# Kernel optimization log

Measured on AMD Instinct MI355X. Metric: run time of the kernel, lower is better.

The kernel has to match this reference:

```python
import jax, jax.numpy as jnp
import numpy as np

DIM = 512
WINDOW = 8
HEADS = 16
HEAD_DIM = DIM // HEADS
SIGMA = 0.39
B = 2048
N = WINDOW * WINDOW


def gaussian_kernel(window_size, sigma):
    """Row-normalised Gaussian attention mask K_sigma (M^2 x M^2)."""
    c = jnp.arange(window_size, dtype=jnp.float32)
    gy, gx = jnp.meshgrid(c, c, indexing='ij')
    pos = jnp.stack([gy.flatten(), gx.flatten()], -1)  # [M^2, 2]
    diff = pos[None, :, :] - pos[:, None, :]           # [M^2, M^2, 2]
    K = jnp.exp(-(diff ** 2).sum(-1) / (2.0 * sigma ** 2))
    return K / K.sum(-1, keepdims=True)


def setup_inputs() -> dict:
    key = jax.random.key(0)
    k1, k2, k3, k4, k5 = jax.random.split(key, 5)
    x = jax.random.normal(k1, (B, N, DIM), dtype=jnp.float32)
    # spectral_norm at inference is just a fixed scaling of the weight; we
    # model the (already-normalised) weights as plain dense params.
    w_qkv = jax.random.normal(k2, (DIM, 3 * DIM), dtype=jnp.float32) * (DIM ** -0.5)
    b_qkv = jax.random.normal(k3, (3 * DIM,), dtype=jnp.float32) * 0.02
    w_proj = jax.random.normal(k4, (DIM, DIM), dtype=jnp.float32) * (DIM ** -0.5)
    b_proj = jax.random.normal(k5, (DIM,), dtype=jnp.float32) * 0.02
    return {"x": x, "w_qkv": w_qkv, "b_qkv": b_qkv, "w_proj": w_proj, "b_proj": b_proj}


def reference(x, w_qkv, b_qkv, w_proj, b_proj):
    Bb, Nn, C = x.shape
    scale = HEAD_DIM ** -0.5
    qkv = (x @ w_qkv + b_qkv).reshape(Bb, Nn, 3, HEADS, HEAD_DIM)
    qkv = jnp.transpose(qkv, (2, 0, 3, 1, 4))  # [3, B, H, N, D]
    q, k, v = qkv[0], qkv[1], qkv[2]
    attn = jnp.einsum('bhnd,bhmd->bhnm', q, k) * scale  # [B, H, N, N]
    K_s = gaussian_kernel(WINDOW, SIGMA)                 # [N, N]
    attn = jax.nn.softmax(attn * K_s, axis=-1)
    out = jnp.einsum('bhnm,bhmd->bhnd', attn, v)         # [B, H, N, D]
    out = jnp.transpose(out, (0, 2, 1, 3)).reshape(Bb, Nn, C)
    return out @ w_proj + b_proj
```

## Files before the change

### kernel.cpp

```cpp
#include <hip/hip_runtime.h>
#include <hip/hip_bf16.h>
#include <stdint.h>

typedef __bf16 bf16;
typedef __bf16 bf16x8 __attribute__((ext_vector_type(8)));
typedef float f32x4 __attribute__((ext_vector_type(4)));
typedef unsigned short u16t;
typedef unsigned int u32t;

#define MFMA16(a, b, c) __builtin_amdgcn_mfma_f32_16x16x32_bf16((a), (b), (c), 0, 0, 0)

typedef const void __attribute__((address_space(1))) cg_void;
typedef void __attribute__((address_space(3))) lds_void;
#define GLL16(g, l) __builtin_amdgcn_global_load_lds((cg_void*)(g), (lds_void*)(l), 16, 0, 0)
#define VWAIT(n) asm volatile("s_waitcnt vmcnt(" #n ")" ::: "memory")

#define OFF_FLAG   0
#define OFF_BQKV   256
#define OFF_BPROJ  6400
#define OFF_WQKVT  8448
#define OFF_WPROJT 1581312
#define OFF_QKV    2105600
#define OFF_ATTN   404758784
#define OFF_XB     404758784

__global__ __launch_bounds__(256) void k_detect(const u16t* x, u32t* flag) {
    __shared__ int cnt;
    if (threadIdx.x == 0) cnt = 0;
    __syncthreads();
    u16t h = x[threadIdx.x * 2];
    int e = (h >> 7) & 0xFF;
    int ok = (h == 0) || (e >= 100 && e <= 134);
    atomicAdd(&cnt, ok);
    __syncthreads();
    if (threadIdx.x == 0) flag[0] = (cnt >= 200) ? 1u : 0u;
}

__global__ __launch_bounds__(256) void k_cvt(const float* x, bf16* xb, const u32t* flagp) {
    if (flagp[0]) return;
    const size_t TOT = (size_t)131072 * 512;
    size_t i = (size_t)(blockIdx.x * 256 + threadIdx.x) * 8;
    const size_t stride = (size_t)gridDim.x * 256 * 8;
    for (; i < TOT; i += stride) {
        float4 v0 = *(const float4*)(x + i);
        float4 v1 = *(const float4*)(x + i + 4);
        bf16x8 h;
        h[0] = (bf16)v0.x; h[1] = (bf16)v0.y; h[2] = (bf16)v0.z; h[3] = (bf16)v0.w;
        h[4] = (bf16)v1.x; h[5] = (bf16)v1.y; h[6] = (bf16)v1.z; h[7] = (bf16)v1.w;
        *(bf16x8*)(xb + i) = h;
    }
}

template <int N>
__global__ __launch_bounds__(256) void k_trans(const void* W, bf16* Wt, const u32t* flagp) {
    __shared__ float T[64][65];
    const int isbf = (int)flagp[0];
    const int n0 = blockIdx.x * 64, k0 = blockIdx.y * 64;
    const int t = threadIdx.x;
    const int lc = t & 63, lr = t >> 6;
#pragma unroll
    for (int rr = 0; rr < 16; ++rr) {
        int row = rr * 4 + lr;
        size_t g = (size_t)(k0 + row) * N + n0 + lc;
        float v = isbf ? (float)((const bf16*)W)[g] : ((const float*)W)[g];
        T[row][lc] = v;
    }
    __syncthreads();
#pragma unroll
    for (int rr = 0; rr < 16; ++rr) {
        int row = rr * 4 + lr;
        Wt[(size_t)(n0 + row) * 512 + k0 + lc] = (bf16)T[lc][row];
    }
}

__global__ __launch_bounds__(256) void k_bias(const void* b_qkv, const void* b_proj,
                                              const u32t* flagp, char* ws) {
    float* bq = (float*)(ws + OFF_BQKV);
    float* bp = (float*)(ws + OFF_BPROJ);
    const int isbf = (int)flagp[0];
    int gid = blockIdx.x * 256 + threadIdx.x;
    if (gid < 1536)
        bq[gid] = isbf ? (float)((const bf16*)b_qkv)[gid] : ((const float*)b_qkv)[gid];
    else if (gid < 2048) {
        int o = gid - 1536;
        bp[o] = isbf ? (float)((const bf16*)b_proj)[o] : ((const float*)b_proj)[o];
    }
}

template <int NTOT>
__global__ __launch_bounds__(512, 2) void k_gemm(const void* Ax, const bf16* Axb, const bf16* Bt,
                                                 const float* bias, void* Cp,
                                                 const u32t* flagp, int omode) {
    __shared__ __align__(16) u16t As[2 * 16384];
    __shared__ __align__(16) u16t Bs[2 * 16384];
    constexpr int NBN = NTOT / 256;
    const int isbf = (int)flagp[0];
    const int out_bf16 = (omode == 1) || isbf;
    const bf16* Ab = isbf ? (const bf16*)Ax : Axb;

    const int t = threadIdx.x;
    const int w = t >> 6, lane = t & 63;
    const int ln = lane & 15, qd = lane >> 4;
    const int wm = w >> 2, wn = w & 3;

    const int flat = blockIdx.x;
    const int xcd = flat & 7, slot = flat >> 3;
    const int n_idx = slot % NBN, grp = slot / NBN;
    const int m0 = (grp * 8 + xcd) * 256;
    const int n0 = n_idx * 256;

    const int l8 = lane >> 3, pc = lane & 7;
    const int cs8 = (pc ^ l8) * 8;
    u32t aoff[2][2], boff[2][2];
    int adst[2][2], bdst[2][2];
#pragma unroll
    for (int s = 0; s < 2; ++s)
#pragma unroll
        for (int q2 = 0; q2 < 2; ++q2) {
            int rA = q2 * 128 + s * 64 + w * 8;
            aoff[s][q2] = (u32t)(m0 + rA + l8) * 512 + cs8;
            adst[s][q2] = rA * 64;
            int rB = (q2 * 2 + (w >> 2)) * 64 + s * 32 + (w & 3) * 8;
            boff[s][q2] = (u32t)(n0 + rB + l8) * 512 + cs8;
            bdst[s][q2] = rB * 64;
        }

    const int p0 = (qd ^ (ln & 7)) * 8;
    int abase[4], bbase[2];
#pragma unroll
    for (int i = 0; i < 4; ++i) abase[i] = (wm * 128 + i * 16 + ln) * 64 + p0;
#pragma unroll
    for (int j = 0; j < 2; ++j) bbase[j] = (wn * 64 + j * 16 + ln) * 64 + p0;

    f32x4 acc[8][4];
    f32x4 zero = {0.f, 0.f, 0.f, 0.f};
#pragma unroll
    for (int i = 0; i < 8; ++i)
#pragma unroll
        for (int j = 0; j < 4; ++j) acc[i][j] = zero;

    auto stageA = [&](int s, int buf, int kt) {
#pragma unroll
        for (int q2 = 0; q2 < 2; ++q2)
            GLL16(Ab + aoff[s][q2] + kt * 64, &As[buf * 16384 + adst[s][q2]]);
    };
    auto stageB = [&](int s, int buf, int kt) {
#pragma unroll
        for (int q2 = 0; q2 < 2; ++q2)
            GLL16(Bt + boff[s][q2] + kt * 64, &Bs[buf * 16384 + bdst[s][q2]]);
    };

#define PH(BUF, QM, QN, STG, WAITOP)                                             \
    {                                                                            \
        bf16x8 af[4][2], bv[2][2];                                               \
        const u16t* Ap = &As[(BUF) * 16384 + (QM) * 4096];                       \
        const u16t* Bp = &Bs[(BUF) * 16384 + (QN) * 2048];                       \
        _Pragma("unroll") for (int i = 0; i < 4; ++i) {                          \
            af[i][0] = *(const bf16x8*)(const void*)&Ap[abase[i]];               \
            af[i][1] = *(const bf16x8*)(const void*)&Ap[abase[i] ^ 32];          \
        }                                                                        \
        _Pragma("unroll") for (int j = 0; j < 2; ++j) {                          \
            bv[j][0] = *(const bf16x8*)(const void*)&Bp[bbase[j]];               \
            bv[j][1] = *(const bf16x8*)(const void*)&Bp[bbase[j] ^ 32];          \
        }                                                                        \
        STG;                                                                     \
        WAITOP;                                                                  \
        __builtin_amdgcn_s_barrier();                                            \
        __builtin_amdgcn_s_setprio(1);                                           \
        _Pragma("unroll") for (int i = 0; i < 4; ++i)                            \
            _Pragma("unroll") for (int j = 0; j < 2; ++j) {                      \
                acc[(QM) * 4 + i][(QN) * 2 + j] =                                \
                    MFMA16(af[i][0], bv[j][0], acc[(QM) * 4 + i][(QN) * 2 + j]); \
                acc[(QM) * 4 + i][(QN) * 2 + j] =                                \
                    MFMA16(af[i][1], bv[j][1], acc[(QM) * 4 + i][(QN) * 2 + j]); \
            }                                                                    \
        __builtin_amdgcn_s_setprio(0);                                           \
        __builtin_amdgcn_s_barrier();                                            \
    }

    stageA(0, 0, 0);
    stageB(0, 0, 0);
    stageB(1, 0, 0);
    stageA(1, 0, 0);
    VWAIT(4);
    __builtin_amdgcn_s_barrier();

    for (int kt = 0; kt < 7; ++kt) {
        const int buf = kt & 1, nb = buf ^ 1, k1 = kt + 1;
        PH(buf, 0, 0, stageA(0, nb, k1), VWAIT(4));
        PH(buf, 0, 1, stageB(0, nb, k1), VWAIT(4));
        PH(buf, 1, 0, stageB(1, nb, k1), VWAIT(6));
        PH(buf, 1, 1, stageA(1, nb, k1), VWAIT(4));
    }
    PH(1, 0, 0, (void)0, VWAIT(2));
    PH(1, 0, 1, (void)0, VWAIT(0));
    PH(1, 1, 0, (void)0, (void)0);
    PH(1, 1, 1, (void)0, (void)0);
#undef PH

    float bj[4];
#pragma unroll
    for (int j = 0; j < 4; ++j) bj[j] = bias[n0 + wn * 64 + j * 16 + ln];

    if (out_bf16) {
        bf16* C = (bf16*)Cp;
#pragma unroll
        for (int i = 0; i < 8; ++i)
#pragma unroll
            for (int j = 0; j < 4; ++j)
#pragma unroll
                for (int rr = 0; rr < 4; ++rr) {
                    size_t row = (size_t)m0 + wm * 128 + i * 16 + qd * 4 + rr;
                    int col = n0 + wn * 64 + j * 16 + ln;
                    C[row * NTOT + col] = (bf16)(acc[i][j][rr] + bj[j]);
                }
    } else {
        float* C = (float*)Cp;
#pragma unroll
        for (int i = 0; i < 8; ++i)
#pragma unroll
            for (int j = 0; j < 4; ++j)
#pragma unroll
                for (int rr = 0; rr < 4; ++rr) {
                    size_t row = (size_t)m0 + wm * 128 + i * 16 + qd * 4 + rr;
                    int col = n0 + wn * 64 + j * 16 + ln;
                    C[row * NTOT + col] = acc[i][j][rr] + bj[j];
                }
    }
}

__global__ __launch_bounds__(256) void k_attn(const bf16* qkv, bf16* attn) {
    __shared__ __align__(16) bf16 P[4][64 * 72];
    __shared__ __align__(16) u16t Vs[4][2048];
    const int t = threadIdx.x;
    const int w = t >> 6, lane = t & 63;
    const int ln = lane & 15, qd = lane >> 4, q8 = qd * 8;
    const int flat = blockIdx.x;
    const int xcd = flat & 7, slot = flat >> 3;
    const int sub = slot & 3, grp = slot >> 2;
    const int b = grp * 8 + xcd;
    const int h = sub * 4 + w;
    const size_t rowbase = (size_t)b * 64 * 1536;
    const int colq = h * 32 + q8;

    bf16x8 aq[4], bk[4];
#pragma unroll
    for (int i = 0; i < 4; ++i)
        aq[i] = *(const bf16x8*)(qkv + rowbase + (size_t)(i * 16 + ln) * 1536 + colq);
#pragma unroll
    for (int j = 0; j < 4; ++j)
        bk[j] = *(const bf16x8*)(qkv + rowbase + (size_t)(j * 16 + ln) * 1536 + 512 + colq);

#pragma unroll
    for (int q = 0; q < 4; ++q) {
        int r = q * 16 + (lane >> 2), pc = lane & 3;
        int c = pc ^ (((r >> 3) ^ r) & 3);
        GLL16(qkv + rowbase + (size_t)r * 1536 + 1024 + h * 32 + c * 8, &Vs[w][q * 512]);
    }

    f32x4 zero = {0.f, 0.f, 0.f, 0.f};
    f32x4 s[4][4];
#pragma unroll
    for (int i = 0; i < 4; ++i)
#pragma unroll
        for (int j = 0; j < 4; ++j) s[i][j] = MFMA16(aq[i], bk[j], zero);

    const float INV2S2 = 3.28731097961867f;
    {
        int c = lane & 7;
        float S1 = 0.f;
#pragma unroll
        for (int c2 = 0; c2 < 8; ++c2) {
            int d = c - c2;
            S1 += __expf(-(float)(d * d) * INV2S2);
        }
        float invS1 = 1.0f / S1;
        const int ymb = ln >> 3, xm = ln & 7, yq = qd >> 1, xq = (qd & 1) * 4;
        float FY[4][4], FX[4];
#pragma unroll
        for (int i = 0; i < 4; ++i) {
            int yn = 2 * i + yq;
            float g = __shfl(invS1, yn, 64);
#pragma unroll
            for (int j = 0; j < 4; ++j) {
                int dy = yn - (2 * j + ymb);
                FY[i][j] = __expf(-(float)(dy * dy) * INV2S2) * g;
            }
        }
#pragma unroll
        for (int rr = 0; rr < 4; ++rr) {
            int xn = xq + rr;
            int dx = xn - xm;
            FX[rr] = __expf(-(float)(dx * dx) * INV2S2) * __shfl(invS1, xn, 64);
        }

        const float SCALE = 0.17677669529663687f;
#pragma unroll
        for (int i = 0; i < 4; ++i)
#pragma unroll
            for (int rr = 0; rr < 4; ++rr) {
                float lj[4];
                float mx = -1e30f;
#pragma unroll
                for (int j = 0; j < 4; ++j) {
                    lj[j] = s[i][j][rr] * SCALE * FY[i][j] * FX[rr];
                    mx = fmaxf(mx, lj[j]);
                }
                mx = fmaxf(mx, __shfl_xor(mx, 1));
                mx = fmaxf(mx, __shfl_xor(mx, 2));
                mx = fmaxf(mx, __shfl_xor(mx, 4));
                mx = fmaxf(mx, __shfl_xor(mx, 8));
                float sum = 0.f;
#pragma unroll
                for (int j = 0; j < 4; ++j) {
                    lj[j] = __expf(lj[j] - mx);
                    sum += lj[j];
                }
                sum += __shfl_xor(sum, 1);
                sum += __shfl_xor(sum, 2);
                sum += __shfl_xor(sum, 4);
                sum += __shfl_xor(sum, 8);
                float inv = 1.0f / sum;
                int n = i * 16 + qd * 4 + rr;
#pragma unroll
                for (int j = 0; j < 4; ++j)
                    P[w][n * 72 + j * 16 + ln] = (bf16)(lj[j] * inv);
            }
    }

    VWAIT(0);

    f32x4 o[4][2];
#pragma unroll
    for (int i = 0; i < 4; ++i) {
        o[i][0] = zero;
        o[i][1] = zero;
    }
#pragma unroll
    for (int kc = 0; kc < 64; kc += 32) {
        bf16x8 bv[2];
#pragma unroll
        for (int j2 = 0; j2 < 2; ++j2) {
            int cc = j2 * 2 + (ln >> 3);
#pragma unroll
            for (int jj = 0; jj < 8; ++jj) {
                int rv = kc + q8 + jj;
                bv[j2][jj] = *(const bf16*)&Vs[w][rv * 32 + (cc ^ (((rv >> 3) ^ rv) & 3)) * 8 + (ln & 7)];
            }
        }
#pragma unroll
        for (int i = 0; i < 4; ++i) {
            bf16x8 ap = *(const bf16x8*)(void*)&P[w][(i * 16 + ln) * 72 + kc + q8];
#pragma unroll
            for (int j2 = 0; j2 < 2; ++j2) o[i][j2] = MFMA16(ap, bv[j2], o[i][j2]);
        }
    }
#pragma unroll
    for (int i = 0; i < 4; ++i)
#pragma unroll
        for (int j2 = 0; j2 < 2; ++j2)
#pragma unroll
            for (int rr = 0; rr < 4; ++rr)
                attn[((size_t)b * 64 + i * 16 + qd * 4 + rr) * 512 + h * 32 + j2 * 16 + ln] =
                    (bf16)(o[i][j2][rr]);
}

extern "C" void kernel_launch(void* const* d_in, const int* in_sizes, int n_in,
                              void* d_out, int out_size, void* d_ws, size_t ws_size,
                              hipStream_t stream) {
    const void* x = d_in[0];
    const void* w_qkv = d_in[1];
    const void* b_qkv = d_in[2];
    const void* w_proj = d_in[3];
    const void* b_proj = d_in[4];
    char* ws = (char*)d_ws;
    u32t* flag = (u32t*)(ws + OFF_FLAG);
    bf16* wqkvT = (bf16*)(ws + OFF_WQKVT);
    bf16* wprojT = (bf16*)(ws + OFF_WPROJT);
    float* bq = (float*)(ws + OFF_BQKV);
    float* bp = (float*)(ws + OFF_BPROJ);
    bf16* qkv = (bf16*)(ws + OFF_QKV);
    bf16* attn = (bf16*)(ws + OFF_ATTN);
    bf16* xb = (bf16*)(ws + OFF_XB);

    k_detect<<<1, 256, 0, stream>>>((const u16t*)x, flag);
    k_cvt<<<2048, 256, 0, stream>>>((const float*)x, xb, flag);
    k_trans<1536><<<dim3(24, 8), 256, 0, stream>>>(w_qkv, wqkvT, flag);
    k_trans<512><<<dim3(8, 8), 256, 0, stream>>>(w_proj, wprojT, flag);
    k_bias<<<8, 256, 0, stream>>>(b_qkv, b_proj, flag, ws);
    k_gemm<1536><<<3072, 512, 0, stream>>>(x, xb, wqkvT, bq, qkv, flag, 1);
    k_attn<<<8192, 256, 0, stream>>>(qkv, attn);
    k_gemm<512><<<1024, 512, 0, stream>>>((const void*)attn, attn, wprojT, bp, d_out, flag, 2);
}
```

Measured before the change: 1.029 ms.

## Fuse QKV projection GEMM with windowed attention in one kernel

Permutes the QKV weight columns and bias so that each 192-wide output tile holds the Q, K and V of two heads. A new fused kernel runs the QKV GEMM for a 256-token by 192-column tile, writes the biased results into LDS in a swizzled per-window layout, then runs softmax attention for 4 windows by 2 heads directly from LDS. This removes the global write and reread of the large intermediate QKV tensor and one kernel launch. The cost is a narrower GEMM N-tile with 3 fragments per wave, higher LDS use, and an attention stage that runs after the GEMM with no overlap.

```diff
diff --git a/kernel.cpp b/kernel.cpp
--- a/kernel.cpp
+++ b/kernel.cpp
@@ -23,6 +23,7 @@
 #define OFF_QKV    2105600
 #define OFF_ATTN   404758784
 #define OFF_XB     404758784
+
 
 __global__ __launch_bounds__(256) void k_detect(const u16t* x, u32t* flag) {
     __shared__ int cnt;
@@ -51,7 +52,7 @@
     }
 }
 
-template <int N>
+template <int N, bool PERM>
 __global__ __launch_bounds__(256) void k_trans(const void* W, bf16* Wt, const u32t* flagp) {
     __shared__ float T[64][65];
     const int isbf = (int)flagp[0];
@@ -61,7 +62,13 @@
 #pragma unroll
     for (int rr = 0; rr < 16; ++rr) {
         int row = rr * 4 + lr;
-        size_t g = (size_t)(k0 + row) * N + n0 + lc;
+        int col = n0 + lc;
+        int srcc = col;
+        if (PERM) {
+            int h = col / 96, r = col % 96;
+            srcc = (r >> 5) * 512 + h * 32 + (r & 31);
+        }
+        size_t g = (size_t)(k0 + row) * N + srcc;
         float v = isbf ? (float)((const bf16*)W)[g] : ((const float*)W)[g];
         T[row][lc] = v;
     }
@@ -79,9 +86,11 @@
     float* bp = (float*)(ws + OFF_BPROJ);
     const int isbf = (int)flagp[0];
     int gid = blockIdx.x * 256 + threadIdx.x;
-    if (gid < 1536)
-        bq[gid] = isbf ? (float)((const bf16*)b_qkv)[gid] : ((const float*)b_qkv)[gid];
-    else if (gid < 2048) {
+    if (gid < 1536) {
+        int h = gid / 96, r = gid % 96;
+        int src = (r >> 5) * 512 + h * 32 + (r & 31);
+        bq[gid] = isbf ? (float)((const bf16*)b_qkv)[src] : ((const float*)b_qkv)[src];
+    } else if (gid < 2048) {
         int o = gid - 1536;
         bp[o] = isbf ? (float)((const bf16*)b_proj)[o] : ((const float*)b_proj)[o];
     }
@@ -229,140 +238,257 @@
     }
 }
 
-__global__ __launch_bounds__(256) void k_attn(const bf16* qkv, bf16* attn) {
-    __shared__ __align__(16) bf16 P[4][64 * 72];
-    __shared__ __align__(16) u16t Vs[4][2048];
+__global__ __launch_bounds__(512, 2) void k_fused(const void* Ax, const bf16* Axb,
+                                                  const bf16* Bt, const float* bias,
+                                                  bf16* attnout, const u32t* flagp) {
+    __shared__ __align__(16) u16t pool[57344];
+    const int isbf = (int)flagp[0];
+    const bf16* Ab = isbf ? (const bf16*)Ax : Axb;
+
     const int t = threadIdx.x;
     const int w = t >> 6, lane = t & 63;
     const int ln = lane & 15, qd = lane >> 4, q8 = qd * 8;
+    const int wm = w >> 2, wn = w & 3;
+
     const int flat = blockIdx.x;
     const int xcd = flat & 7, slot = flat >> 3;
-    const int sub = slot & 3, grp = slot >> 2;
-    const int b = grp * 8 + xcd;
-    const int h = sub * 4 + w;
-    const size_t rowbase = (size_t)b * 64 * 1536;
-    const int colq = h * 32 + q8;
-
-    bf16x8 aq[4], bk[4];
-#pragma unroll
-    for (int i = 0; i < 4; ++i)
-        aq[i] = *(const bf16x8*)(qkv + rowbase + (size_t)(i * 16 + ln) * 1536 + colq);
-#pragma unroll
-    for (int j = 0; j < 4; ++j)
-        bk[j] = *(const bf16x8*)(qkv + rowbase + (size_t)(j * 16 + ln) * 1536 + 512 + colq);
-
-#pragma unroll
-    for (int q = 0; q < 4; ++q) {
-        int r = q * 16 + (lane >> 2), pc = lane & 3;
-        int c = pc ^ (((r >> 3) ^ r) & 3);
-        GLL16(qkv + rowbase + (size_t)r * 1536 + 1024 + h * 32 + c * 8, &Vs[w][q * 512]);
-    }
-
+    const int n_idx = slot & 7, grp = slot >> 3;
+    const int m0 = (grp * 8 + xcd) * 256;
+    const int n0 = n_idx * 192;
+
+    const int l8 = lane >> 3, pc = lane & 7;
+    const int cs8 = (pc ^ l8) * 8;
+    u32t aoff[4], boff[3];
+    int adst[4], bdst[3];
+#pragma unroll
+    for (int qa = 0; qa < 4; ++qa) {
+        int row = qa * 64 + w * 8 + l8;
+        aoff[qa] = (u32t)(m0 + row) * 512 + cs8;
+        adst[qa] = (qa * 512 + w * 64) * 8;
+    }
+#pragma unroll
+    for (int qb = 0; qb < 3; ++qb) {
+        int row = qb * 64 + w * 8 + l8;
+        boff[qb] = (u32t)(n0 + row) * 512 + cs8;
+        bdst[qb] = (qb * 512 + w * 64) * 8;
+    }
+
+    const int swz = (qd ^ (ln & 7)) * 8;
+    int afo[2][4], bfo[3];
+#pragma unroll
+    for (int qm = 0; qm < 2; ++qm)
+#pragma unroll
+        for (int i = 0; i < 4; ++i)
+            afo[qm][i] = (wm * 128 + qm * 64 + i * 16 + ln) * 64 + swz;
+#pragma unroll
+    for (int j = 0; j < 3; ++j) bfo[j] = (wn * 48 + j * 16 + ln) * 64 + swz;
+
+    f32x4 acc[8][3];
     f32x4 zero = {0.f, 0.f, 0.f, 0.f};
-    f32x4 s[4][4];
-#pragma unroll
-    for (int i = 0; i < 4; ++i)
-#pragma unroll
-        for (int j = 0; j < 4; ++j) s[i][j] = MFMA16(aq[i], bk[j], zero);
-
-    const float INV2S2 = 3.28731097961867f;
-    {
-        int c = lane & 7;
-        float S1 = 0.f;
-#pragma unroll
-        for (int c2 = 0; c2 < 8; ++c2) {
-            int d = c - c2;
-            S1 += __expf(-(float)(d * d) * INV2S2);
-        }
-        float invS1 = 1.0f / S1;
-        const int ymb = ln >> 3, xm = ln & 7, yq = qd >> 1, xq = (qd & 1) * 4;
-        float FY[4][4], FX[4];
-#pragma unroll
-        for (int i = 0; i < 4; ++i) {
-            int yn = 2 * i + yq;
-            float g = __shfl(invS1, yn, 64);
-#pragma unroll
-            for (int j = 0; j < 4; ++j) {
-                int dy = yn - (2 * j + ymb);
-                FY[i][j] = __expf(-(float)(dy * dy) * INV2S2) * g;
+#pragma unroll
+    for (int i = 0; i < 8; ++i)
+#pragma unroll
+        for (int j = 0; j < 3; ++j) acc[i][j] = zero;
+
+    auto stA = [&](int qa, int buf, int kt) {
+        GLL16(Ab + aoff[qa] + kt * 64, &pool[buf * 16384 + adst[qa]]);
+    };
+    auto stB = [&](int qb, int buf, int kt) {
+        GLL16(Bt + boff[qb] + kt * 64, &pool[32768 + buf * 12288 + bdst[qb]]);
+    };
+
+#define PHF(BUF, QM, KK, STG, WAITOP)                                           \
+    {                                                                           \
+        bf16x8 af[4], bv[3];                                                    \
+        _Pragma("unroll") for (int i = 0; i < 4; ++i)                           \
+            af[i] = *(const bf16x8*)(const void*)                               \
+                &pool[(BUF) * 16384 + (afo[QM][i] ^ ((KK) * 32))];              \
+        _Pragma("unroll") for (int j = 0; j < 3; ++j)                           \
+            bv[j] = *(const bf16x8*)(const void*)                               \
+                &pool[32768 + (BUF) * 12288 + (bfo[j] ^ ((KK) * 32))];          \
+        STG;                                                                    \
+        WAITOP;                                                                 \
+        __builtin_amdgcn_s_barrier();                                           \
+        __builtin_amdgcn_s_setprio(1);                                          \
+        _Pragma("unroll") for (int i = 0; i < 4; ++i)                           \
+            _Pragma("unroll") for (int j = 0; j < 3; ++j)                       \
+                acc[(QM) * 4 + i][j] = MFMA16(af[i], bv[j], acc[(QM) * 4 + i][j]); \
+        __builtin_amdgcn_s_setprio(0);                                          \
+        __builtin_amdgcn_s_barrier();                                           \
+    }
+
+    stA(0, 0, 0); stA(2, 0, 0);
+    stB(0, 0, 0); stB(1, 0, 0); stB(2, 0, 0);
+    stA(1, 0, 0); stA(3, 0, 0);
+    VWAIT(2);
+    __builtin_amdgcn_s_barrier();
+
+    for (int kt = 0; kt < 7; ++kt) {
+        const int buf = kt & 1, nb = buf ^ 1, k1 = kt + 1;
+        PHF(buf, 0, 0, (stA(0, nb, k1), stA(2, nb, k1)), (void)0);
+        PHF(buf, 0, 1, (stB(0, nb, k1), stB(1, nb, k1)), VWAIT(4));
+        PHF(buf, 1, 0, (stB(2, nb, k1), stA(1, nb, k1)), (void)0);
+        PHF(buf, 1, 1, (stA(3, nb, k1)), VWAIT(2));
+    }
+    PHF(1, 0, 0, (void)0, (void)0);
+    PHF(1, 0, 1, (void)0, VWAIT(0));
+    PHF(1, 1, 0, (void)0, (void)0);
+    PHF(1, 1, 1, (void)0, (void)0);
+#undef PHF
+
+    float bj[3];
+#pragma unroll
+    for (int j = 0; j < 3; ++j) bj[j] = bias[n0 + wn * 48 + j * 16 + ln];
+
+#pragma unroll
+    for (int i = 0; i < 8; ++i) {
+        int win = wm * 2 + (i >> 2);
+#pragma unroll
+        for (int j = 0; j < 3; ++j) {
+            int base = wn * 48 + j * 16;
+            int hl = base >= 96;
+            int bb = base - hl * 96;
+            int part = bb >> 5;
+            int d = (bb & 31) + ln;
+            int patch = (win * 2 + hl) * 6656;
+#pragma unroll
+            for (int rr = 0; rr < 4; ++rr) {
+                int tok = (i & 3) * 16 + qd * 4 + rr;
+                bf16 val = (bf16)(acc[i][j][rr] + bj[j]);
+                int idx;
+                if (part == 2)
+                    idx = patch + 4608 + tok * 32 +
+                          (((d >> 3) ^ (((tok >> 3) ^ tok) & 3)) << 3) + (d & 7);
+                else
+                    idx = patch + part * 2048 + tok * 32 +
+                          (((d >> 3) ^ ((tok >> 1) & 3)) << 3) + (d & 7);
+                *(bf16*)&pool[idx] = val;
             }
         }
-#pragma unroll
-        for (int rr = 0; rr < 4; ++rr) {
-            int xn = xq + rr;
-            int dx = xn - xm;
-            FX[rr] = __expf(-(float)(dx * dx) * INV2S2) * __shfl(invS1, xn, 64);
+    }
+    __syncthreads();
+
+    {
+        const int patch = w * 6656;
+        const int win = w >> 1, hl = w & 1;
+        const int hcol = (n_idx * 2 + hl) * 32;
+        const int qswz = (qd ^ ((ln >> 1) & 3)) * 8;
+
+        bf16x8 aq[4], bk[4];
+#pragma unroll
+        for (int i = 0; i < 4; ++i)
+            aq[i] = *(const bf16x8*)(const void*)&pool[patch + (i * 16 + ln) * 32 + qswz];
+#pragma unroll
+        for (int j = 0; j < 4; ++j)
+            bk[j] = *(const bf16x8*)(const void*)&pool[patch + 2048 + (j * 16 + ln) * 32 + qswz];
+
+        f32x4 zro = {0.f, 0.f, 0.f, 0.f};
+        f32x4 s[4][4];
+#pragma unroll
+        for (int i = 0; i < 4; ++i)
+#pragma unroll
+            for (int j = 0; j < 4; ++j) s[i][j] = MFMA16(aq[i], bk[j], zro);
+
+        const float INV2S2 = 3.28731097961867f;
+        {
+            int c = lane & 7;
+            float S1 = 0.f;
+#pragma unroll
+            for (int c2 = 0; c2 < 8; ++c2) {
+                int dd = c - c2;
+                S1 += __expf(-(float)(dd * dd) * INV2S2);
+            }
+            float invS1 = 1.0f / S1;
+            const int ymb = ln >> 3, xm = ln & 7, yq = qd >> 1, xq = (qd & 1) * 4;
+            float FY[4][4], FX[4];
+#pragma unroll
+            for (int i = 0; i < 4; ++i) {
+                int yn = 2 * i + yq;
+                float g = __shfl(invS1, yn, 64);
+#pragma unroll
+                for (int j = 0; j < 4; ++j) {
+                    int dy = yn - (2 * j + ymb);
+                    FY[i][j] = __expf(-(float)(dy * dy) * INV2S2) * g;
+                }
+            }
+#pragma unroll
+            for (int rr = 0; rr < 4; ++rr) {
+                int xn = xq + rr;
+                int dx = xn - xm;
+                FX[rr] = __expf(-(float)(dx * dx) * INV2S2) * __shfl(invS1, xn, 64);
+            }
+
+            const float SCALE = 0.17677669529663687f;
+#pragma unroll
+            for (int i = 0; i < 4; ++i)
+#pragma unroll
+                for (int rr = 0; rr < 4; ++rr) {
+                    float lj[4];
+                    float mx = -1e30f;
+#pragma unroll
+                    for (int j = 0; j < 4; ++j) {
+                        lj[j] = s[i][j][rr] * SCALE * FY[i][j] * FX[rr];
+                        mx = fmaxf(mx, lj[j]);
+                    }
+                    mx = fmaxf(mx, __shfl_xor(mx, 1));
+                    mx = fmaxf(mx, __shfl_xor(mx, 2));
+                    mx = fmaxf(mx, __shfl_xor(mx, 4));
+                    mx = fmaxf(mx, __shfl_xor(mx, 8));
+                    float sum = 0.f;
+#pragma unroll
+                    for (int j = 0; j < 4; ++j) {
+                        lj[j] = __expf(lj[j] - mx);
+                        sum += lj[j];
+                    }
+                    sum += __shfl_xor(sum, 1);
+                    sum += __shfl_xor(sum, 2);
+                    sum += __shfl_xor(sum, 4);
+                    sum += __shfl_xor(sum, 8);
+                    float inv = 1.0f / sum;
+                    int n = i * 16 + qd * 4 + rr;
+#pragma unroll
+                    for (int j = 0; j < 4; ++j) {
+                        bf16 pv = (bf16)(lj[j] * inv);
+                        *(bf16*)&pool[patch + n * 72 + j * 16 + ln] = pv;
+                    }
+                }
         }
 
-        const float SCALE = 0.17677669529663687f;
-#pragma unroll
-        for (int i = 0; i < 4; ++i)
-#pragma unroll
-            for (int rr = 0; rr < 4; ++rr) {
-                float lj[4];
-                float mx = -1e30f;
-#pragma unroll
-                for (int j = 0; j < 4; ++j) {
-                    lj[j] = s[i][j][rr] * SCALE * FY[i][j] * FX[rr];
-                    mx = fmaxf(mx, lj[j]);
+        f32x4 o[4][2];
+#pragma unroll
+        for (int i = 0; i < 4; ++i) {
+            o[i][0] = zro;
+            o[i][1] = zro;
+        }
+#pragma unroll
+        for (int kc = 0; kc < 64; kc += 32) {
+            bf16x8 bv2[2];
+#pragma unroll
+            for (int j2 = 0; j2 < 2; ++j2) {
+                int cc = j2 * 2 + (ln >> 3);
+#pragma unroll
+                for (int jj = 0; jj < 8; ++jj) {
+                    int rv = kc + q8 + jj;
+                    bv2[j2][jj] = *(const bf16*)&pool[patch + 4608 + rv * 32 +
+                                                     ((cc ^ (((rv >> 3) ^ rv) & 3)) << 3) + (ln & 7)];
                 }
-                mx = fmaxf(mx, __shfl_xor(mx, 1));
-                mx = fmaxf(mx, __shfl_xor(mx, 2));
-                mx = fmaxf(mx, __shfl_xor(mx, 4));
-                mx = fmaxf(mx, __shfl_xor(mx, 8));
-                float sum = 0.f;
-#pragma unroll
-                for (int j = 0; j < 4; ++j) {
-                    lj[j] = __expf(lj[j] - mx);
-                    sum += lj[j];
-                }
-                sum += __shfl_xor(sum, 1);
-                sum += __shfl_xor(sum, 2);
-                sum += __shfl_xor(sum, 4);
-                sum += __shfl_xor(sum, 8);
-                float inv = 1.0f / sum;
-                int n = i * 16 + qd * 4 + rr;
-#pragma unroll
-                for (int j = 0; j < 4; ++j)
-                    P[w][n * 72 + j * 16 + ln] = (bf16)(lj[j] * inv);
             }
-    }
-
-    VWAIT(0);
-
-    f32x4 o[4][2];
-#pragma unroll
-    for (int i = 0; i < 4; ++i) {
-        o[i][0] = zero;
-        o[i][1] = zero;
-    }
-#pragma unroll
-    for (int kc = 0; kc < 64; kc += 32) {
-        bf16x8 bv[2];
-#pragma unroll
-        for (int j2 = 0; j2 < 2; ++j2) {
-            int cc = j2 * 2 + (ln >> 3);
-#pragma unroll
-            for (int jj = 0; jj < 8; ++jj) {
-                int rv = kc + q8 + jj;
-                bv[j2][jj] = *(const bf16*)&Vs[w][rv * 32 + (cc ^ (((rv >> 3) ^ rv) & 3)) * 8 + (ln & 7)];
+#pragma unroll
+            for (int i = 0; i < 4; ++i) {
+                bf16x8 ap = *(const bf16x8*)(const void*)&pool[patch + (i * 16 + ln) * 72 + kc + q8];
+#pragma unroll
+                for (int j2 = 0; j2 < 2; ++j2) o[i][j2] = MFMA16(ap, bv2[j2], o[i][j2]);
             }
         }
 #pragma unroll
-        for (int i = 0; i < 4; ++i) {
-            bf16x8 ap = *(const bf16x8*)(void*)&P[w][(i * 16 + ln) * 72 + kc + q8];
-#pragma unroll
-            for (int j2 = 0; j2 < 2; ++j2) o[i][j2] = MFMA16(ap, bv[j2], o[i][j2]);
-        }
-    }
-#pragma unroll
-    for (int i = 0; i < 4; ++i)
-#pragma unroll
-        for (int j2 = 0; j2 < 2; ++j2)
-#pragma unroll
-            for (int rr = 0; rr < 4; ++rr)
-                attn[((size_t)b * 64 + i * 16 + qd * 4 + rr) * 512 + h * 32 + j2 * 16 + ln] =
-                    (bf16)(o[i][j2][rr]);
+        for (int i = 0; i < 4; ++i)
+#pragma unroll
+            for (int j2 = 0; j2 < 2; ++j2)
+#pragma unroll
+                for (int rr = 0; rr < 4; ++rr)
+                    attnout[((size_t)m0 + win * 64 + i * 16 + qd * 4 + rr) * 512 +
+                            hcol + j2 * 16 + ln] = (bf16)(o[i][j2][rr]);
+    }
 }
 
 extern "C" void kernel_launch(void* const* d_in, const int* in_sizes, int n_in,
@@ -379,16 +505,14 @@
     bf16* wprojT = (bf16*)(ws + OFF_WPROJT);
     float* bq = (float*)(ws + OFF_BQKV);
     float* bp = (float*)(ws + OFF_BPROJ);
-    bf16* qkv = (bf16*)(ws + OFF_QKV);
-    bf16* attn = (bf16*)(ws + OFF_ATTN);
+    bf16* attnout = (bf16*)(ws + OFF_QKV);
     bf16* xb = (bf16*)(ws + OFF_XB);
 
     k_detect<<<1, 256, 0, stream>>>((const u16t*)x, flag);
     k_cvt<<<2048, 256, 0, stream>>>((const float*)x, xb, flag);
-    k_trans<1536><<<dim3(24, 8), 256, 0, stream>>>(w_qkv, wqkvT, flag);
-    k_trans<512><<<dim3(8, 8), 256, 0, stream>>>(w_proj, wprojT, flag);
+    k_trans<1536, true><<<dim3(24, 8), 256, 0, stream>>>(w_qkv, wqkvT, flag);
+    k_trans<512, false><<<dim3(8, 8), 256, 0, stream>>>(w_proj, wprojT, flag);
     k_bias<<<8, 256, 0, stream>>>(b_qkv, b_proj, flag, ws);
-    k_gemm<1536><<<3072, 512, 0, stream>>>(x, xb, wqkvT, bq, qkv, flag, 1);
-    k_attn<<<8192, 256, 0, stream>>>(qkv, attn);
-    k_gemm<512><<<1024, 512, 0, stream>>>((const void*)attn, attn, wprojT, bp, d_out, flag, 2);
-}
+    k_fused<<<4096, 512, 0, stream>>>(x, xb, wqkvT, bq, attnout, flag);
+    k_gemm<512><<<1024, 512, 0, stream>>>((const void*)attnout, attnout, wprojT, bp, d_out, flag, 2);
+}
```

After: 953.2 us. 1.08x faster.
